# Kernel optimization log

Measured on AMD Instinct MI355X. Metric: run time of the kernel, lower is better.

Reference implementation:

```python
import jax, jax.numpy as jnp
import numpy as np
import math

DIM = 1024
NUM_HEADS = 16
HEAD_DIM = DIM // NUM_HEADS
EPS = 1e-6
DILATED = 2
WINDOW = 2  # window_size init arg; actual window = L * WINDOW per side


def setup_inputs() -> dict:
    key = jax.random.key(0)
    ks = jax.random.split(key, 14)
    B, S = 1, 8704
    x = jax.random.normal(ks[0], (B, S, DIM), jnp.float32)
    ang = jax.random.uniform(ks[1], (S, HEAD_DIM // 2), jnp.float32, -jnp.pi, jnp.pi)
    freqs_cos = jnp.cos(ang)
    freqs_sin = jnp.sin(ang)
    def lin(k):
        return 0.02 * jax.random.normal(k, (DIM, DIM), jnp.float32)
    def bias(k):
        return 0.01 * jax.random.normal(k, (DIM,), jnp.float32)
    return {
        'x': x, 'freqs_cos': freqs_cos, 'freqs_sin': freqs_sin,
        'wq': lin(ks[2]), 'bq': bias(ks[3]),
        'wk': lin(ks[4]), 'bk': bias(ks[5]),
        'wv': lin(ks[6]), 'bv': bias(ks[7]),
        'wo': lin(ks[8]), 'bo': bias(ks[9]),
        'gq': 1.0 + 0.02 * jax.random.normal(ks[10], (DIM,), jnp.float32),
        'gk': 1.0 + 0.02 * jax.random.normal(ks[11], (DIM,), jnp.float32),
        'f': 34, 'L': 256,
    }


def rmsnorm(h, g):
    return h * jax.lax.rsqrt(jnp.mean(h * h, axis=-1, keepdims=True) + EPS) * g


def rope(h, cos, sin):
    # h: [B,S,D] viewed as interleaved complex pairs per head, rotated by unit freqs
    B, S, D = h.shape
    hp = h.reshape(B, S, NUM_HEADS, HEAD_DIM // 2, 2)
    a, b = hp[..., 0], hp[..., 1]
    c = cos[None, :, None, :]
    s = sin[None, :, None, :]
    ra = a * c - b * s
    rb = a * s + b * c
    return jnp.stack([ra, rb], axis=-1).reshape(B, S, D)


def windowed_attention(q, k, v, w):
    # sliding-window attention: query i attends keys j with |i-j| <= w (inclusive)
    B, S, D = q.shape
    H, hd = NUM_HEADS, HEAD_DIM
    def heads(t):
        return t.reshape(B, S, H, hd).transpose(0, 2, 1, 3)  # [B,H,S,hd]
    qh, kh, vh = heads(q), heads(k), heads(v)
    C = w  # block size == window -> only 3 neighbor key blocks per query block
    pad = (-S) % C
    Sp = S + pad
    nb = Sp // C
    def blocks(t):
        return jnp.pad(t, ((0, 0), (0, 0), (0, pad), (0, 0))).reshape(B, H, nb, C, hd)
    qb = blocks(qh)
    def win(t):
        tb = jnp.pad(blocks(t), ((0, 0), (0, 0), (1, 1), (0, 0), (0, 0)))
        return jnp.concatenate([tb[:, :, i:i + nb] for i in range(3)], axis=3)  # [B,H,nb,3C,hd]
    kw_, vw_ = win(kh), win(vh)
    scores = jnp.einsum('bhnqd,bhnkd->bhnqk', qb, kw_) * (1.0 / math.sqrt(hd))
    qi = jnp.arange(nb)[:, None, None] * C + jnp.arange(C)[None, :, None]      # [nb,C,1]
    kj = (jnp.arange(nb)[:, None, None] - 1) * C + jnp.arange(3 * C)[None, None, :]  # [nb,1,3C]
    valid = (kj >= 0) & (kj < S) & (qi - kj <= w) & (kj - qi <= w)
    scores = jnp.where(valid, scores, -1e9)
    p = jax.nn.softmax(scores, axis=-1)
    o = jnp.einsum('bhnqk,bhnkd->bhnqd', p, vw_)
    return o.reshape(B, H, Sp, hd)[:, :, :S].transpose(0, 2, 1, 3).reshape(B, S, D)


def reference(x, freqs_cos, freqs_sin, wq, bq, wk, bk, wv, bv, wo, bo, gq, gk, f, L):
    B, S, D = x.shape
    q = rope(rmsnorm(x @ wq + bq, gq), freqs_cos, freqs_sin)
    k = rope(rmsnorm(x @ wk + bk, gk), freqs_cos, freqs_sin)
    v = x @ wv + bv
    w = L * WINDOW
    use_dilated = DILATED > 1 and S // (DILATED * L) > 1
    if use_dilated:
        blk = DILATED * L
        pad_len = blk - S % blk  # == blk when S % blk == 0 (faithful to torch code)
        Sp = S + pad_len
        n = Sp // blk
        def padd(t):
            return jnp.pad(t, ((0, 0), (0, pad_len), (0, 0)))
        def dil(t):
            # 'b (n d l) c -> (b d) (n l) c'
            return t.reshape(B, n, DILATED, L, D).transpose(0, 2, 1, 3, 4).reshape(B * DILATED, n * L, D)
        q, k, v = dil(padd(q)), dil(padd(k)), dil(padd(v))
    o = windowed_attention(q, k, v, w)
    out = o @ wo + bo
    if use_dilated:
        # '(b d) (n l) c -> b (n d l) c', then drop pad
        out = out.reshape(B, DILATED, n, L, D).transpose(0, 2, 1, 3, 4).reshape(B, n * DILATED * L, D)
        out = out[:, :S]
    return out
```

## Files before the change

kernel.cpp:

```cpp
#include <hip/hip_runtime.h>
#include <hip/hip_bf16.h>
#include <stdint.h>

#define DIM 1024
#define NH 16
#define HD 64
#define S_ORIG 8704
#define WIN 512

typedef __attribute__((ext_vector_type(8))) short short8;
typedef __attribute__((ext_vector_type(4))) float f32x4;

__device__ __forceinline__ float bf2f(unsigned short u) {
    return __uint_as_float(((unsigned int)u) << 16);
}
__device__ __forceinline__ unsigned short f2bf(float f) {
    unsigned int x = __float_as_uint(f);
    unsigned int r = x + 0x7fffu + ((x >> 16) & 1u);
    return (unsigned short)(r >> 16);
}
__device__ __forceinline__ unsigned int cvtpk(float lo, float hi) {
    unsigned int r;
    asm("v_cvt_pk_bf16_f32 %0, %1, %2" : "=v"(r) : "v"(lo), "v"(hi));
    return r;
}
__device__ __forceinline__ float fexp2(float x) {
#if __has_builtin(__builtin_amdgcn_exp2f)
    return __builtin_amdgcn_exp2f(x);
#else
    float r;
    asm("v_exp_f32 %0, %1" : "=v"(r) : "v"(x));
    return r;
#endif
}

#define GLD_LDS(gptr, lptr) \
    __builtin_amdgcn_global_load_lds((const __attribute__((address_space(1))) void*)(gptr), \
                                     (__attribute__((address_space(3))) void*)(lptr), 16, 0, 0)

#define FBAR() do { __asm__ volatile("" ::: "memory"); \
                    __builtin_amdgcn_s_barrier(); \
                    __asm__ volatile("" ::: "memory"); } while (0)

__global__ __launch_bounds__(256) void prep(const float* __restrict__ x,
                                            unsigned short* __restrict__ xb,
                                            const float* __restrict__ w0,
                                            const float* __restrict__ w1,
                                            const float* __restrict__ w2,
                                            const float* __restrict__ w3,
                                            unsigned short* __restrict__ wt) {
    __shared__ float ts[64][65];
    const int bx = blockIdx.x;
    const int t = threadIdx.x;
    if (bx < 8704) {
        int i = (bx * 256 + t) * 4;
        float4 v = *(const float4*)(x + i);
        ushort4 o;
        o.x = f2bf(v.x); o.y = f2bf(v.y); o.z = f2bf(v.z); o.w = f2bf(v.w);
        *(ushort4*)(xb + i) = o;
        return;
    }
    const int b = bx - 8704;
    const int z = b >> 8;
    const int rem = b & 255;
    const int kb = (rem >> 4) * 64, nb = (rem & 15) * 64;
    const float* w = z == 0 ? w0 : z == 1 ? w1 : z == 2 ? w2 : w3;
    unsigned short* o = wt + (size_t)z * DIM * DIM;
    const int c = t & 63, r4 = t >> 6;
#pragma unroll
    for (int rr = 0; rr < 16; rr++) {
        int row = rr * 4 + r4;
        ts[row][c] = w[(size_t)(kb + row) * DIM + nb + c];
    }
    __syncthreads();
#pragma unroll
    for (int rr = 0; rr < 16; rr++) {
        int nl = rr * 4 + r4;
        o[(size_t)(nb + nl) * DIM + kb + c] = f2bf(ts[c][nl]);
    }
}

template <int OUTF32>
__global__ __launch_bounds__(256) void gemm_bf16(const unsigned short* __restrict__ A,
                                                 const unsigned short* __restrict__ Bt,
                                                 const float* __restrict__ b0,
                                                 const float* __restrict__ b1,
                                                 const float* __restrict__ b2,
                                                 void* __restrict__ Cout) {
    __shared__ __align__(16) unsigned short As[128 * 32];
    __shared__ __align__(16) unsigned short Bs[128 * 32];
    const int z = blockIdx.z;
    const unsigned short* B = Bt + (size_t)z * DIM * DIM;
    const float* bias = z == 0 ? b0 : (z == 1 ? b1 : b2);
    const int m0 = blockIdx.x * 128, n0 = blockIdx.y * 128;
    const int tid = threadIdx.x;
    const int lane = tid & 63, wv = tid >> 6;
    const int wr = wv >> 1, wc = wv & 1;
    const int quad = lane >> 4, r = lane & 15;

    f32x4 acc[4][4];
#pragma unroll
    for (int i = 0; i < 4; i++)
#pragma unroll
        for (int j = 0; j < 4; j++)
#pragma unroll
            for (int t4 = 0; t4 < 4; t4++) acc[i][j][t4] = 0.0f;

    const unsigned short* a_base = A + (size_t)m0 * DIM;
    const unsigned short* b_base = B + (size_t)n0 * DIM;
    const int c0 = wv * 128 + lane;
    const int r0 = c0 >> 2, o0 = (((c0 & 3) ^ ((c0 >> 3) & 3))) * 8;
    const int c1 = c0 + 64;
    const int r1 = c1 >> 2, o1 = (((c1 & 3) ^ ((c1 >> 3) & 3))) * 8;
    unsigned short* lA0 = &As[(size_t)(wv * 128) * 8];
    unsigned short* lA1 = &As[(size_t)(wv * 128 + 64) * 8];
    unsigned short* lB0 = &Bs[(size_t)(wv * 128) * 8];
    unsigned short* lB1 = &Bs[(size_t)(wv * 128 + 64) * 8];

    const int jsw = (quad ^ ((r >> 1) & 3)) * 8;

    for (int k0 = 0; k0 < DIM; k0 += 32) {
        __syncthreads();
        GLD_LDS(a_base + (size_t)r0 * DIM + k0 + o0, lA0);
        GLD_LDS(a_base + (size_t)r1 * DIM + k0 + o1, lA1);
        GLD_LDS(b_base + (size_t)r0 * DIM + k0 + o0, lB0);
        GLD_LDS(b_base + (size_t)r1 * DIM + k0 + o1, lB1);
        __syncthreads();
        short8 af[4], bfr[4];
#pragma unroll
        for (int i = 0; i < 4; i++)
            af[i] = *(const short8*)&As[(wr * 64 + i * 16 + r) * 32 + jsw];
#pragma unroll
        for (int j = 0; j < 4; j++)
            bfr[j] = *(const short8*)&Bs[(wc * 64 + j * 16 + r) * 32 + jsw];
#pragma unroll
        for (int i = 0; i < 4; i++)
#pragma unroll
            for (int j = 0; j < 4; j++)
                acc[i][j] = __builtin_amdgcn_mfma_f32_16x16x32_bf16(af[i], bfr[j], acc[i][j], 0, 0, 0);
    }

#pragma unroll
    for (int i = 0; i < 4; i++) {
        const int row = m0 + wr * 64 + i * 16 + quad * 4;
#pragma unroll
        for (int j = 0; j < 4; j++) {
            const int col = n0 + wc * 64 + j * 16 + r;
            const float bvl = bias[col];
#pragma unroll
            for (int t4 = 0; t4 < 4; t4++) {
                float vv = acc[i][j][t4] + bvl;
                if (OUTF32) {
                    ((float*)Cout)[(size_t)(row + t4) * DIM + col] = vv;
                } else {
                    ((unsigned short*)Cout)[(size_t)z * S_ORIG * DIM + (size_t)(row + t4) * DIM + col] = f2bf(vv);
                }
            }
        }
    }
}

__global__ __launch_bounds__(256) void norm_rope(unsigned short* __restrict__ hq,
                                                 unsigned short* __restrict__ hk,
                                                 const float* __restrict__ gq,
                                                 const float* __restrict__ gk,
                                                 const float* __restrict__ fcos,
                                                 const float* __restrict__ fsin) {
    const int z = blockIdx.y;
    unsigned short* h = z == 0 ? hq : hk;
    const float* g = z == 0 ? gq : gk;
    const int w = threadIdx.x >> 6, lane = threadIdx.x & 63;
    const int srow = blockIdx.x * 4 + w;
    unsigned short* hp = h + (size_t)srow * DIM;
    const int p0 = lane * 8, p1 = 512 + lane * 8;

    union { int4 i4; unsigned short u[8]; } r0, r1, o0, o1;
    r0.i4 = *(const int4*)(hp + p0);
    r1.i4 = *(const int4*)(hp + p1);
    float v[16];
#pragma unroll
    for (int j = 0; j < 8; j++) { v[j] = bf2f(r0.u[j]); v[8 + j] = bf2f(r1.u[j]); }

    float ss = 0.0f;
#pragma unroll
    for (int j = 0; j < 16; j++) ss += v[j] * v[j];
#pragma unroll
    for (int off = 1; off < 64; off <<= 1) ss += __shfl_xor(ss, off, 64);
    const float rinv = rsqrtf(ss * (1.0f / DIM) + 1e-6f);

    float4 ga = *(const float4*)(g + p0), gb = *(const float4*)(g + p0 + 4);
    float4 gc = *(const float4*)(g + p1), gd = *(const float4*)(g + p1 + 4);
    const float* gg[4] = {&ga.x, &gb.x, &gc.x, &gd.x};
#pragma unroll
    for (int q4 = 0; q4 < 4; q4++)
#pragma unroll
        for (int j = 0; j < 4; j++) v[q4 * 4 + j] *= rinv * gg[q4][j];

    const int i0 = (p0 & 63) >> 1;
    float4 cs = *(const float4*)(fcos + (size_t)srow * 32 + i0);
    float4 sn = *(const float4*)(fsin + (size_t)srow * 32 + i0);
    const float* cp = &cs.x;
    const float* sp = &sn.x;
#pragma unroll
    for (int seg = 0; seg < 2; seg++) {
        unsigned short* uo = seg == 0 ? o0.u : o1.u;
#pragma unroll
        for (int pr = 0; pr < 4; pr++) {
            const float a = v[seg * 8 + pr * 2], b = v[seg * 8 + pr * 2 + 1];
            uo[pr * 2]     = f2bf(a * cp[pr] - b * sp[pr]);
            uo[pr * 2 + 1] = f2bf(a * sp[pr] + b * cp[pr]);
        }
    }
    *(int4*)(hp + p0) = o0.i4;
    *(int4*)(hp + p1) = o1.i4;
}

__device__ __forceinline__ void qstep(const unsigned short* __restrict__ Ks,
                                      const unsigned short* __restrict__ Vt,
                                      unsigned short* __restrict__ pw,
                                      int jsw0, int jsw1, int quad, int r16,
                                      int kbase, int qi, bool edge,
                                      const short8* __restrict__ qf,
                                      f32x4* __restrict__ oacc, float& lsum) {
    f32x4 sv[4];
#pragma unroll
    for (int nt = 0; nt < 4; nt++) {
        const int row = (nt * 16 + r16) * 64;
        short8 k0f = *(const short8*)&Ks[row + jsw0];
        short8 k1f = *(const short8*)&Ks[row + jsw1];
        f32x4 a = {0.0f, 0.0f, 0.0f, 0.0f};
        a = __builtin_amdgcn_mfma_f32_16x16x32_bf16(k0f, qf[0], a, 0, 0, 0);
        a = __builtin_amdgcn_mfma_f32_16x16x32_bf16(k1f, qf[1], a, 0, 0, 0);
        sv[nt] = a;
    }
#pragma unroll
    for (int nt = 0; nt < 4; nt++) {
        float p[4];
#pragma unroll
        for (int rr = 0; rr < 4; rr++) {
            float e = fexp2(sv[nt][rr]);
            if (edge) {
                const int kj = kbase + nt * 16 + quad * 4 + rr;
                const int dl = qi - kj;
                if (dl > WIN || dl < -WIN) e = 0.0f;
            }
            p[rr] = e;
        }
        lsum += (p[0] + p[1]) + (p[2] + p[3]);
        uint2 pk;
        pk.x = cvtpk(p[0], p[1]);
        pk.y = cvtpk(p[2], p[3]);
        *(uint2*)&pw[r16 * 72 + nt * 16 + quad * 4] = pk;
    }
    __asm__ volatile("s_waitcnt lgkmcnt(0)" ::: "memory");
    short8 pf0 = *(const short8*)&pw[r16 * 72 + quad * 8];
    short8 pf1 = *(const short8*)&pw[r16 * 72 + 32 + quad * 8];
#pragma unroll
    for (int nt = 0; nt < 4; nt++) {
        short8 v0f = *(const short8*)&Vt[(nt * 16 + r16) * 72 + quad * 8];
        short8 v1f = *(const short8*)&Vt[(nt * 16 + r16) * 72 + 32 + quad * 8];
        oacc[nt] = __builtin_amdgcn_mfma_f32_16x16x32_bf16(v0f, pf0, oacc[nt], 0, 0, 0);
        oacc[nt] = __builtin_amdgcn_mfma_f32_16x16x32_bf16(v1f, pf1, oacc[nt], 0, 0, 0);
    }
}

__device__ __forceinline__ void pack_write_v(unsigned short* __restrict__ Vt,
                                             int4 a0i, int4 a1i, int vt_d0, int vt_kk) {
    union { int4 i4; unsigned int w[4]; } a0, a1;
    a0.i4 = a0i; a1.i4 = a1i;
#pragma unroll
    for (int dw = 0; dw < 4; dw++) {
        unsigned int lo = __builtin_amdgcn_perm(a1.w[dw], a0.w[dw], 0x05040100u);
        unsigned int hi = __builtin_amdgcn_perm(a1.w[dw], a0.w[dw], 0x07060302u);
        *(unsigned int*)&Vt[(vt_d0 + dw * 2) * 72 + vt_kk] = lo;
        *(unsigned int*)&Vt[(vt_d0 + dw * 2 + 1) * 72 + vt_kk] = hi;
    }
}

__global__ __launch_bounds__(256) void attn(const unsigned short* __restrict__ qkv,
                                            unsigned short* __restrict__ ob) {
    __shared__ __align__(16) unsigned short Ks[2][64 * 64];
    __shared__ __align__(16) unsigned short Vt[64 * 72];
    __shared__ __align__(16) unsigned short Ps[4][16 * 72];

    const int head = blockIdx.x >> 1;
    const int d = blockIdx.x & 1;
    const int t0 = blockIdx.y * 2, t1 = t0 + 1;
    const int tid = threadIdx.x;
    const int lane = tid & 63, wv = tid >> 6;
    const int quad = lane >> 4, r16 = lane & 15;

    const unsigned short* qb = qkv;
    const unsigned short* kb = qkv + (size_t)S_ORIG * DIM;
    const unsigned short* vb = qkv + (size_t)2 * S_ORIG * DIM;

    const int qi0 = t0 * 64 + wv * 16 + r16;
    const int qi1 = qi0 + 64;
    const int og_q0 = ((qi0 >> 8) << 9) + d * 256 + (qi0 & 255);
    const int og_q1 = ((qi1 >> 8) << 9) + d * 256 + (qi1 & 255);
    short8 qf0[2], qf1[2];
    {
        const float QSC = 0.125f * 1.44269504088896f;
        const unsigned short* qr0 = qb + (size_t)og_q0 * DIM + head * HD + quad * 8;
        const unsigned short* qr1 = qb + (size_t)og_q1 * DIM + head * HD + quad * 8;
#pragma unroll
        for (int c = 0; c < 2; c++) {
            union { int4 i4; unsigned short u[8]; short8 s8; } i0v, i1v, a0v, a1v;
            i0v.i4 = *(const int4*)(qr0 + c * 32);
            i1v.i4 = *(const int4*)(qr1 + c * 32);
#pragma unroll
            for (int j = 0; j < 8; j++) {
                a0v.u[j] = f2bf(bf2f(i0v.u[j]) * QSC);
                a1v.u[j] = f2bf(bf2f(i1v.u[j]) * QSC);
            }
            qf0[c] = a0v.s8;
            qf1[c] = a1v.s8;
        }
    }

    f32x4 oacc0[4], oacc1[4];
    float lsum0 = 0.0f, lsum1 = 0.0f;
#pragma unroll
    for (int nt = 0; nt < 4; nt++)
#pragma unroll
        for (int rr = 0; rr < 4; rr++) { oacc0[nt][rr] = 0.0f; oacc1[nt][rr] = 0.0f; }

    const int kt_lo = (t0 - 8 > 0) ? (t0 - 8) : 0;
    const int kt_hi = (t1 + 8 < 67) ? (t1 + 8) : 67;

    const int krow0 = tid >> 3;
    const int kgc = ((tid & 7) ^ (krow0 & 7)) * 8;

    const int vt_kk = (tid & 31) * 2, vt_d0 = (tid >> 5) * 8;

    const int jsw0 = (quad ^ (r16 & 7)) * 8;
    const int jsw1 = jsw0 ^ 32;

    unsigned short* pw = &Ps[wv][0];

#define ISSUE_K(kbase_, bufb_) do {                                              \
        const int kj0_ = (kbase_) + krow0;                                       \
        const int ok0_ = ((kj0_ >> 8) << 9) + d * 256 + (kj0_ & 255);            \
        GLD_LDS(kb + (size_t)ok0_ * DIM + head * HD + kgc, (bufb_) + wv * 512);  \
        const int kj1_ = kj0_ + 32;                                              \
        const int ok1_ = ((kj1_ >> 8) << 9) + d * 256 + (kj1_ & 255);            \
        GLD_LDS(kb + (size_t)ok1_ * DIM + head * HD + kgc, (bufb_) + 2048 + wv * 512); \
    } while (0)

#define LOAD_V(kbase_, a0_, a1_) do {                                            \
        const int kj_ = (kbase_) + vt_kk;                                        \
        const int ok_ = ((kj_ >> 8) << 9) + d * 256 + (kj_ & 255);               \
        (a0_) = *(const int4*)(vb + (size_t)ok_ * DIM + head * HD + vt_d0);      \
        (a1_) = *(const int4*)(vb + (size_t)(ok_ + 1) * DIM + head * HD + vt_d0);\
    } while (0)

    ISSUE_K(kt_lo * 64, &Ks[0][0]);
    int4 vc0, vc1;
    LOAD_V(kt_lo * 64, vc0, vc1);

    int cur = 0;
    for (int kt = kt_lo; kt <= kt_hi; kt++) {
        const int kbase = kt * 64;
        FBAR();

        const int knb = ((kt < kt_hi) ? (kt + 1) : kt_hi) * 64;
        ISSUE_K(knb, &Ks[cur ^ 1][0]);
        int4 vn0, vn1;
        LOAD_V(knb, vn0, vn1);

        __asm__ volatile("s_waitcnt vmcnt(4)" ::: "memory");
        __builtin_amdgcn_sched_barrier(0);

        pack_write_v(&Vt[0], vc0, vc1, vt_d0, vt_kk);
        __asm__ volatile("s_waitcnt lgkmcnt(0)" ::: "memory");
        FBAR();

        if (kt <= t0 + 8)
            qstep(&Ks[cur][0], Vt, pw, jsw0, jsw1, quad, r16, kbase, qi0,
                  (kt == t0 - 8) || (kt == t0 + 8), qf0, oacc0, lsum0);
        if (kt >= t1 - 8)
            qstep(&Ks[cur][0], Vt, pw, jsw0, jsw1, quad, r16, kbase, qi1,
                  (kt == t1 - 8) || (kt == t1 + 8), qf1, oacc1, lsum1);

        vc0 = vn0; vc1 = vn1;
        cur ^= 1;
    }
#undef ISSUE_K
#undef LOAD_V

    __asm__ volatile("" :: "v"(vc0.x), "v"(vc0.y), "v"(vc0.z), "v"(vc0.w),
                          "v"(vc1.x), "v"(vc1.y), "v"(vc1.z), "v"(vc1.w));
    __asm__ volatile("s_waitcnt vmcnt(0)" ::: "memory");

    lsum0 += __shfl_xor(lsum0, 16, 64);
    lsum0 += __shfl_xor(lsum0, 32, 64);
    lsum1 += __shfl_xor(lsum1, 16, 64);
    lsum1 += __shfl_xor(lsum1, 32, 64);
    {
        const int cnt0 = (qi0 + WIN < 4607 ? qi0 + WIN : 4607) - 4351;
        if (cnt0 > 0) lsum0 += (float)cnt0;
        const int cnt1 = (qi1 + WIN < 4607 ? qi1 + WIN : 4607) - 4351;
        if (cnt1 > 0) lsum1 += (float)cnt1;
    }
    const float linv0 = 1.0f / lsum0;
    const float linv1 = 1.0f / lsum1;

#pragma unroll
    for (int nt = 0; nt < 4; nt++) {
        ushort4 o0, o1;
        o0.x = f2bf(oacc0[nt][0] * linv0);
        o0.y = f2bf(oacc0[nt][1] * linv0);
        o0.z = f2bf(oacc0[nt][2] * linv0);
        o0.w = f2bf(oacc0[nt][3] * linv0);
        *(ushort4*)&ob[(size_t)og_q0 * DIM + head * HD + nt * 16 + quad * 4] = o0;
        o1.x = f2bf(oacc1[nt][0] * linv1);
        o1.y = f2bf(oacc1[nt][1] * linv1);
        o1.z = f2bf(oacc1[nt][2] * linv1);
        o1.w = f2bf(oacc1[nt][3] * linv1);
        *(ushort4*)&ob[(size_t)og_q1 * DIM + head * HD + nt * 16 + quad * 4] = o1;
    }
}

extern "C" void kernel_launch(void* const* d_in, const int* in_sizes, int n_in,
                              void* d_out, int out_size, void* d_ws, size_t ws_size,
                              hipStream_t stream) {
    const float* x    = (const float*)d_in[0];
    const float* fcos = (const float*)d_in[1];
    const float* fsin = (const float*)d_in[2];
    const float* wq   = (const float*)d_in[3];
    const float* bq   = (const float*)d_in[4];
    const float* wk   = (const float*)d_in[5];
    const float* bk   = (const float*)d_in[6];
    const float* wv   = (const float*)d_in[7];
    const float* bv   = (const float*)d_in[8];
    const float* wo   = (const float*)d_in[9];
    const float* bo   = (const float*)d_in[10];
    const float* gq   = (const float*)d_in[11];
    const float* gk   = (const float*)d_in[12];

    char* ws = (char*)d_ws;
    unsigned short* xb = (unsigned short*)(ws);
    unsigned short* wt = (unsigned short*)(ws + 17825792);
    unsigned short* h  = (unsigned short*)(ws + 26214400);
    unsigned short* ob = (unsigned short*)(ws + 79691776);
    float* outp = (float*)d_out;

    prep<<<9728, 256, 0, stream>>>(x, xb, wq, wk, wv, wo, wt);
    gemm_bf16<0><<<dim3(68, 8, 3), 256, 0, stream>>>(xb, wt, bq, bk, bv, (void*)h);
    norm_rope<<<dim3(2176, 2), 256, 0, stream>>>(h, h + (size_t)S_ORIG * DIM, gq, gk, fcos, fsin);
    attn<<<dim3(32, 34), 256, 0, stream>>>(h, ob);
    gemm_bf16<1><<<dim3(68, 8, 1), 256, 0, stream>>>(ob, wt + (size_t)3 * DIM * DIM, bo, bo, bo, (void*)outp);
}
```

Baseline: 312.2 us.

## Triple-buffer LDS in bf16 GEMM to overlap global loads with MFMA

Replaces the single-buffered LDS tile loop in the projection GEMM with a three-stage ring of LDS buffers. Global-to-LDS loads for step k+2 are issued before computing step k, and explicit vmcnt waits plus barriers control ordering. The aim is to hide global memory latency behind MFMA work. In exchange LDS use triples, which may reduce occupancy, and correctness depends on the hand-tuned waitcnt values.

```diff
diff --git a/kernel.cpp b/kernel.cpp
--- a/kernel.cpp
+++ b/kernel.cpp
@@ -80,6 +80,24 @@
     }
 }
 
+__device__ __forceinline__ void gemm_step(const unsigned short* __restrict__ pa,
+                                          const unsigned short* __restrict__ pb,
+                                          int wr, int wc, int r, int jsw,
+                                          f32x4 acc[4][4]) {
+    short8 af[4], bfr[4];
+#pragma unroll
+    for (int i = 0; i < 4; i++)
+        af[i] = *(const short8*)&pa[(wr * 64 + i * 16 + r) * 32 + jsw];
+#pragma unroll
+    for (int j = 0; j < 4; j++)
+        bfr[j] = *(const short8*)&pb[(wc * 64 + j * 16 + r) * 32 + jsw];
+#pragma unroll
+    for (int i = 0; i < 4; i++)
+#pragma unroll
+        for (int j = 0; j < 4; j++)
+            acc[i][j] = __builtin_amdgcn_mfma_f32_16x16x32_bf16(af[i], bfr[j], acc[i][j], 0, 0, 0);
+}
+
 template <int OUTF32>
 __global__ __launch_bounds__(256) void gemm_bf16(const unsigned short* __restrict__ A,
                                                  const unsigned short* __restrict__ Bt,
@@ -87,8 +105,8 @@
                                                  const float* __restrict__ b1,
                                                  const float* __restrict__ b2,
                                                  void* __restrict__ Cout) {
-    __shared__ __align__(16) unsigned short As[128 * 32];
-    __shared__ __align__(16) unsigned short Bs[128 * 32];
+    __shared__ __align__(16) unsigned short As[3][128 * 32];
+    __shared__ __align__(16) unsigned short Bs[3][128 * 32];
     const int z = blockIdx.z;
     const unsigned short* B = Bt + (size_t)z * DIM * DIM;
     const float* bias = z == 0 ? b0 : (z == 1 ? b1 : b2);
@@ -112,33 +130,49 @@
     const int r0 = c0 >> 2, o0 = (((c0 & 3) ^ ((c0 >> 3) & 3))) * 8;
     const int c1 = c0 + 64;
     const int r1 = c1 >> 2, o1 = (((c1 & 3) ^ ((c1 >> 3) & 3))) * 8;
-    unsigned short* lA0 = &As[(size_t)(wv * 128) * 8];
-    unsigned short* lA1 = &As[(size_t)(wv * 128 + 64) * 8];
-    unsigned short* lB0 = &Bs[(size_t)(wv * 128) * 8];
-    unsigned short* lB1 = &Bs[(size_t)(wv * 128 + 64) * 8];
+    const int ld0 = (wv * 128) * 8, ld1 = (wv * 128 + 64) * 8;
 
     const int jsw = (quad ^ ((r >> 1) & 3)) * 8;
 
-    for (int k0 = 0; k0 < DIM; k0 += 32) {
-        __syncthreads();
-        GLD_LDS(a_base + (size_t)r0 * DIM + k0 + o0, lA0);
-        GLD_LDS(a_base + (size_t)r1 * DIM + k0 + o1, lA1);
-        GLD_LDS(b_base + (size_t)r0 * DIM + k0 + o0, lB0);
-        GLD_LDS(b_base + (size_t)r1 * DIM + k0 + o1, lB1);
-        __syncthreads();
-        short8 af[4], bfr[4];
-#pragma unroll
-        for (int i = 0; i < 4; i++)
-            af[i] = *(const short8*)&As[(wr * 64 + i * 16 + r) * 32 + jsw];
-#pragma unroll
-        for (int j = 0; j < 4; j++)
-            bfr[j] = *(const short8*)&Bs[(wc * 64 + j * 16 + r) * 32 + jsw];
-#pragma unroll
-        for (int i = 0; i < 4; i++)
-#pragma unroll
-            for (int j = 0; j < 4; j++)
-                acc[i][j] = __builtin_amdgcn_mfma_f32_16x16x32_bf16(af[i], bfr[j], acc[i][j], 0, 0, 0);
-    }
+#define ISSUE_STEP(k0_, abuf_, bbuf_) do {                                  \
+        GLD_LDS(a_base + (size_t)r0 * DIM + (k0_) + o0, (abuf_) + ld0);     \
+        GLD_LDS(a_base + (size_t)r1 * DIM + (k0_) + o1, (abuf_) + ld1);     \
+        GLD_LDS(b_base + (size_t)r0 * DIM + (k0_) + o0, (bbuf_) + ld0);     \
+        GLD_LDS(b_base + (size_t)r1 * DIM + (k0_) + o1, (bbuf_) + ld1);     \
+    } while (0)
+
+    unsigned short *pa0 = &As[0][0], *pa1 = &As[1][0], *pa2 = &As[2][0];
+    unsigned short *pb0 = &Bs[0][0], *pb1 = &Bs[1][0], *pb2 = &Bs[2][0];
+
+    ISSUE_STEP(0, pa0, pb0);
+    ISSUE_STEP(32, pa1, pb1);
+
+#pragma unroll 3
+    for (int k0 = 0; k0 < DIM - 64; k0 += 32) {
+        FBAR();
+        ISSUE_STEP(k0 + 64, pa2, pb2);
+        __asm__ volatile("s_waitcnt vmcnt(8)" ::: "memory");
+        __builtin_amdgcn_sched_barrier(0);
+        FBAR();
+        gemm_step(pa0, pb0, wr, wc, r, jsw, acc);
+        unsigned short* t;
+        t = pa0; pa0 = pa1; pa1 = pa2; pa2 = t;
+        t = pb0; pb0 = pb1; pb1 = pb2; pb2 = t;
+    }
+    __asm__ volatile("s_waitcnt vmcnt(4)" ::: "memory");
+    __builtin_amdgcn_sched_barrier(0);
+    FBAR();
+    gemm_step(pa0, pb0, wr, wc, r, jsw, acc);
+    {
+        unsigned short* t;
+        t = pa0; pa0 = pa1; pa1 = pa2; pa2 = t;
+        t = pb0; pb0 = pb1; pb1 = pb2; pb2 = t;
+    }
+    __asm__ volatile("s_waitcnt vmcnt(0)" ::: "memory");
+    __builtin_amdgcn_sched_barrier(0);
+    FBAR();
+    gemm_step(pa0, pb0, wr, wc, r, jsw, acc);
+#undef ISSUE_STEP
 
 #pragma unroll
     for (int i = 0; i < 4; i++) {
```

New measurement: 302.6 us. 3.1% less time.
